# Performance work log

Measured on AMD Instinct MI355X. Metric: run time of the kernel, lower is better.

The kernel has to match this reference:

```python
import jax, jax.numpy as jnp
import numpy as np


def setup_inputs() -> dict:
    key = jax.random.key(0)
    ks = jax.random.split(key, 6)
    B, T, D, U = 128, 1024, 256, 256
    x = jax.random.normal(ks[0], (B, T, D), jnp.float32)
    s = lambda k, sh: jax.random.normal(k, sh, jnp.float32) * 0.05
    W_zr = s(ks[1], (D, 2 * U))
    U_zr = s(ks[2], (U, 2 * U))
    # bias_initializer: zeros for update gate, ones for reset gate
    b_zr = jnp.concatenate([jnp.zeros((U,), jnp.float32), jnp.ones((U,), jnp.float32)])
    W_h = s(ks[3], (D, U))
    U_h = s(ks[4], (U, U))
    b_h = jnp.zeros((U,), jnp.float32)
    return {"x": x, "W_zr": W_zr, "U_zr": U_zr, "b_zr": b_zr,
            "W_h": W_h, "U_h": U_h, "b_h": b_h}


def reference(x, W_zr, U_zr, b_zr, W_h, U_h, b_h):
    B, T, D = x.shape
    U = W_h.shape[1]
    # Precompute input-side projections for all timesteps (math-equivalent,
    # batches the per-step Dense(ip) matmuls into two big GEMMs).
    xz = jnp.einsum('btd,de->bte', x, W_zr)   # [B,T,2U]
    xh = jnp.einsum('btd,du->btu', x, W_h)    # [B,T,U]

    def step(h, inp):
        xz_t, xh_t = inp                       # [B,2U], [B,U]
        z = xz_t + h @ U_zr + b_zr
        Z = jax.nn.sigmoid(z[:, :U])           # update gate
        R = jax.nn.sigmoid(z[:, U:2 * U])      # reset gate
        S_ = jnp.tanh(xh_t + (R * h) @ U_h + b_h)
        h_new = (1.0 - Z) * h + Z * S_
        return h_new, None

    h0 = jnp.zeros((B, U), x.dtype)
    h_last, _ = jax.lax.scan(step, h0,
                             (jnp.swapaxes(xz, 0, 1), jnp.swapaxes(xh, 0, 1)))
    # return_sequence=False, return_states=False -> last hidden state [B,U]
    return h_last
```

## Files before the change

### kernel.cpp

```cpp
#include <hip/hip_runtime.h>
#include <hip/hip_bf16.h>
#include <cstdint>
#include <cstddef>

#define B_ 128
#define T_ 1024
#define D_ 256
#define U_ 256

typedef __bf16 bfrag __attribute__((ext_vector_type(8)));
typedef unsigned short us8 __attribute__((ext_vector_type(8)));
typedef unsigned short us4 __attribute__((ext_vector_type(4)));
typedef float f32x4 __attribute__((ext_vector_type(4)));

#define SC_ZR (-1.4426950408889634f)
#define SC_H  (2.8853900817779268f)

__device__ __forceinline__ unsigned short f2bf(float f) {
    unsigned int u = __builtin_bit_cast(unsigned int, f);
    unsigned int r = (u + 0x7fffu + ((u >> 16) & 1u)) >> 16;
    return (unsigned short)r;
}
__device__ __forceinline__ float bf2f(unsigned short h) {
    unsigned int u = ((unsigned int)h) << 16;
    return __builtin_bit_cast(float, u);
}
__device__ __forceinline__ unsigned int pk_bf16(float lo, float hi) {
    unsigned int d;
    asm("v_cvt_pk_bf16_f32 %0, %1, %2" : "=v"(d) : "v"(lo), "v"(hi));
    return d;
}
__device__ __forceinline__ unsigned int pk_hu(float lo, float hi) {
    unsigned int a = __builtin_bit_cast(unsigned int, lo) + 0x8000u;
    unsigned int b = __builtin_bit_cast(unsigned int, hi) + 0x8000u;
#if __has_builtin(__builtin_amdgcn_perm)
    return __builtin_amdgcn_perm(b, a, 0x07060302u);
#else
    return (b & 0xffff0000u) | (a >> 16);
#endif
}

#if __has_builtin(__builtin_amdgcn_exp2f)
__device__ __forceinline__ float fexp2(float x) { return __builtin_amdgcn_exp2f(x); }
#else
__device__ __forceinline__ float fexp2(float x) { return exp2f(x); }
#endif
#if __has_builtin(__builtin_amdgcn_rcpf)
__device__ __forceinline__ float frcp(float x) { return __builtin_amdgcn_rcpf(x); }
#else
__device__ __forceinline__ float frcp(float x) { return 1.0f / x; }
#endif

__device__ __forceinline__ float sigm_pre(float zp) {
    return frcp(1.0f + fexp2(zp));
}
__device__ __forceinline__ float tanh_pre(float sp) {
    return 1.0f - 2.0f * frcp(1.0f + fexp2(sp));
}

#define BARRIER_LGKM() asm volatile("s_waitcnt lgkmcnt(0)\n\ts_barrier" ::: "memory")

#define TSTR (32 * 768 * 4)
#define WTSZ (768 * 256)

__global__ __launch_bounds__(64) void wt_kernel(
    const float* __restrict__ Wzr, const float* __restrict__ Wh,
    unsigned short* __restrict__ Wt, int ncopies)
{
    const int c = blockIdx.x;
    const int lane = threadIdx.x;
    const float* Wp; int ldw, cc;
    if (c < 512) { Wp = Wzr; ldw = 512; cc = c; }
    else         { Wp = Wh;  ldw = 256; cc = c - 512; }
    const float sc = (c < 512) ? SC_ZR : SC_H;
    const int k0 = lane * 4;
    const float a = sc * Wp[(size_t)(k0 + 0) * ldw + cc];
    const float b = sc * Wp[(size_t)(k0 + 1) * ldw + cc];
    const float d = sc * Wp[(size_t)(k0 + 2) * ldw + cc];
    const float e = sc * Wp[(size_t)(k0 + 3) * ldw + cc];
    uint2 u; u.x = pk_bf16(a, b); u.y = pk_bf16(d, e);
    for (int r = 0; r < ncopies; ++r)
        *reinterpret_cast<uint2*>(&Wt[(size_t)r * WTSZ + (size_t)c * 256 + k0]) = u;
}

#define LPA 264

__global__ __launch_bounds__(256, 4) void proj_kernel(
    const float* __restrict__ x, const unsigned short* __restrict__ Wt,
    const float* __restrict__ bzr, const float* __restrict__ bh,
    unsigned short* __restrict__ xzh, size_t wtstride)
{
    const int tid  = threadIdx.x;
    const int lane = tid & 63;
    const int wv   = tid >> 6;
    const int q    = lane >> 4;
    const int c16  = lane & 15;
    const int bb = blockIdx.x >> 8;
    const int tb = blockIdx.x & 255;

    __shared__ __align__(16) unsigned short ldsA[64 * LPA];

    {
        const int r0 = wv * 16;
#pragma unroll
        for (int r = 0; r < 16; ++r) {
            const int row = r0 + r;
            const float* xr = x + (((size_t)(bb * 16 + (row & 15))) * T_
                                   + tb * 4 + (row >> 4)) * D_;
            f32x4 v = *reinterpret_cast<const f32x4*>(xr + lane * 4);
            uint2 u; u.x = pk_bf16(v[0], v[1]); u.y = pk_bf16(v[2], v[3]);
            *reinterpret_cast<uint2*>(&ldsA[row * LPA + lane * 4]) = u;
        }
    }
    __syncthreads();

    const int R0 = (wv >> 1) * 32;
    us8 af[2][8];
#pragma unroll
    for (int m2 = 0; m2 < 2; ++m2)
#pragma unroll
        for (int kk = 0; kk < 8; ++kk)
            af[m2][kk] = *reinterpret_cast<const us8*>(
                &ldsA[(R0 + m2 * 16 + c16) * LPA + kk * 32 + q * 8]);

    const int wn = wv & 1;
    const unsigned short* p0 = Wt + (size_t)bb * wtstride
                               + ((size_t)(wn * 32 + c16) * 256 + q * 8);
    const unsigned short* p1 = p0 + 16 * 256;

#pragma unroll 1
    for (int ch = 0; ch < 12; ++ch) {
        f32x4 acc[2][2] = {};
#pragma unroll
        for (int kk = 0; kk < 8; ++kk) {
            us8 w0 = *reinterpret_cast<const us8*>(p0 + kk * 32);
            us8 w1 = *reinterpret_cast<const us8*>(p1 + kk * 32);
#pragma unroll
            for (int m2 = 0; m2 < 2; ++m2) {
                acc[m2][0] = __builtin_amdgcn_mfma_f32_16x16x32_bf16(
                    __builtin_bit_cast(bfrag, af[m2][kk]), __builtin_bit_cast(bfrag, w0),
                    acc[m2][0], 0, 0, 0);
                acc[m2][1] = __builtin_amdgcn_mfma_f32_16x16x32_bf16(
                    __builtin_bit_cast(bfrag, af[m2][kk]), __builtin_bit_cast(bfrag, w1),
                    acc[m2][1], 0, 0, 0);
            }
        }
#pragma unroll
        for (int n2 = 0; n2 < 2; ++n2) {
            const int gcn = ch * 64 + wn * 32 + n2 * 16 + c16;
            const float bias = (gcn < 512) ? (SC_ZR * bzr[gcn])
                                           : (SC_H * bh[gcn - 512]);
#pragma unroll
            for (int m2 = 0; m2 < 2; ++m2) {
                const int t = tb * 4 + (wv >> 1) * 2 + m2;
                uint2 uu;
                uu.x = pk_bf16(acc[m2][n2][0] + bias, acc[m2][n2][1] + bias);
                uu.y = pk_bf16(acc[m2][n2][2] + bias, acc[m2][n2][3] + bias);
                *reinterpret_cast<uint2*>(
                    &xzh[(((size_t)t * 32 + bb * 4 + q) * 768 + gcn) * 4]) = uu;
            }
        }
        p0 += 64 * 256; p1 += 64 * 256;
    }
}

#define HBP 272

__global__ __launch_bounds__(512, 2) void gru_rec(
    const float* __restrict__ Uzr, const float* __restrict__ Uh,
    const unsigned short* __restrict__ xzh, float* __restrict__ out)
{
    const int tid  = threadIdx.x;
    const int lane = tid & 63;
    const int w    = tid >> 6;
    const int q    = lane >> 4;
    const int c16  = lane & 15;
    const int g    = blockIdx.x;

    __shared__ __align__(16) unsigned short hb[4 * HBP];
    __shared__ __align__(16) unsigned short rhb[4 * HBP];

    us8 wA[4][8];
#pragma unroll
    for (int nt = 0; nt < 4; ++nt) {
        const int col = (nt < 2) ? (w * 32 + nt * 16 + c16)
                                 : (256 + w * 32 + (nt - 2) * 16 + c16);
#pragma unroll
        for (int kk = 0; kk < 8; ++kk) {
            us8 v;
#pragma unroll
            for (int j = 0; j < 8; ++j) {
                const int kr = kk * 32 + q * 4 + (j >> 1) + 16 * (j & 1);
                v[j] = f2bf(SC_ZR * Uzr[(size_t)kr * 512 + col]);
            }
            wA[nt][kk] = v;
        }
    }
    us8 wB[2][8];
#pragma unroll
    for (int nt = 0; nt < 2; ++nt) {
        const int col = w * 32 + nt * 16 + c16;
#pragma unroll
        for (int kk = 0; kk < 8; ++kk) {
            us8 v;
#pragma unroll
            for (int j = 0; j < 8; ++j) {
                const int kr = kk * 32 + q * 4 + (j >> 1) + 16 * (j & 1);
                v[j] = f2bf(SC_H * Uh[(size_t)kr * 256 + col]);
            }
            wB[nt][kk] = v;
        }
    }

    for (int i = tid; i < 4 * HBP; i += 512) { hb[i] = 0; rhb[i] = 0; }
    __syncthreads();

    float h0 = 0.0f, h1 = 0.0f;

    size_t laneA[4], laneB[2];
#pragma unroll
    for (int nt = 0; nt < 4; ++nt) {
        const int col = (nt < 2) ? (w * 32 + nt * 16 + c16)
                                 : (256 + w * 32 + (nt - 2) * 16 + c16);
        laneA[nt] = ((size_t)g * 768 + col) * 4 + q;
    }
#pragma unroll
    for (int nt = 0; nt < 2; ++nt)
        laneB[nt] = ((size_t)g * 768 + 512 + w * 32 + nt * 16 + c16) * 4 + q;

    unsigned short ca[4], cxh[2];
#pragma unroll
    for (int nt = 0; nt < 4; ++nt) ca[nt] = xzh[laneA[nt]];
#pragma unroll
    for (int nt = 0; nt < 2; ++nt) cxh[nt] = xzh[laneB[nt]];

    size_t toff = TSTR;

    const int dwr = q * HBP + w * 32 + 2 * c16;
    const int ard = (c16 >> 2) * HBP + q * 8;

#pragma unroll 1
    for (int t = 0; t < T_; ++t) {
        unsigned short na[4], nxh[2];
#pragma unroll
        for (int nt = 0; nt < 4; ++nt) na[nt] = xzh[laneA[nt] + toff];
#pragma unroll
        for (int nt = 0; nt < 2; ++nt) nxh[nt] = xzh[laneB[nt] + toff];
        if (t < 1022) toff += TSTR;

        f32x4 acc[4];
#pragma unroll
        for (int nt = 0; nt < 4; ++nt) {
            const float v = bf2f(ca[nt]);
            acc[nt][0] = v; acc[nt][1] = v; acc[nt][2] = v; acc[nt][3] = v;
        }
#pragma unroll
        for (int kk = 0; kk < 8; ++kk) {
            bfrag af = __builtin_bit_cast(bfrag,
                *reinterpret_cast<const us8*>(&hb[ard + kk * 32]));
#pragma unroll
            for (int nt = 0; nt < 4; ++nt)
                acc[nt] = __builtin_amdgcn_mfma_f32_16x16x32_bf16(
                    af, __builtin_bit_cast(bfrag, wA[nt][kk]), acc[nt], 0, 0, 0);
        }
        {
            const float r0 = sigm_pre(acc[2][0]);
            const float r1 = sigm_pre(acc[3][0]);
            *reinterpret_cast<unsigned int*>(&rhb[dwr]) = pk_hu(r0 * h0, r1 * h1);
        }
        BARRIER_LGKM();

        f32x4 acc2[2];
#pragma unroll
        for (int nt = 0; nt < 2; ++nt) {
            const float v = bf2f(cxh[nt]);
            acc2[nt][0] = v; acc2[nt][1] = v; acc2[nt][2] = v; acc2[nt][3] = v;
        }
#pragma unroll
        for (int kk = 0; kk < 8; ++kk) {
            bfrag rf = __builtin_bit_cast(bfrag,
                *reinterpret_cast<const us8*>(&rhb[ard + kk * 32]));
#pragma unroll
            for (int nt = 0; nt < 2; ++nt)
                acc2[nt] = __builtin_amdgcn_mfma_f32_16x16x32_bf16(
                    rf, __builtin_bit_cast(bfrag, wB[nt][kk]), acc2[nt], 0, 0, 0);
        }
        {
            const float z0 = sigm_pre(acc[0][0]);
            const float z1 = sigm_pre(acc[1][0]);
            const float s0 = tanh_pre(acc2[0][0]);
            const float s1 = tanh_pre(acc2[1][0]);
            h0 = fmaf(z0, s0 - h0, h0);
            h1 = fmaf(z1, s1 - h1, h1);
            *reinterpret_cast<unsigned int*>(&hb[dwr]) = pk_hu(h0, h1);
        }
#pragma unroll
        for (int nt = 0; nt < 4; ++nt) ca[nt] = na[nt];
#pragma unroll
        for (int nt = 0; nt < 2; ++nt) cxh[nt] = nxh[nt];
        BARRIER_LGKM();
    }

    out[(size_t)(g * 4 + q) * 256 + w * 32 + c16] = h0;
    out[(size_t)(g * 4 + q) * 256 + w * 32 + 16 + c16] = h1;
}

extern "C" void kernel_launch(void* const* d_in, const int* in_sizes, int n_in,
                              void* d_out, int out_size, void* d_ws, size_t ws_size,
                              hipStream_t stream) {
    const float* x   = (const float*)d_in[0];
    const float* Wzr = (const float*)d_in[1];
    const float* Uzr = (const float*)d_in[2];
    const float* bzr = (const float*)d_in[3];
    const float* Wh  = (const float*)d_in[4];
    const float* Uh  = (const float*)d_in[5];
    const float* bh  = (const float*)d_in[6];
    float* out = (float*)d_out;

    const size_t xzhbytes = (size_t)T_ * TSTR * 2;
    const size_t wtbytes  = (size_t)WTSZ * 2;
    int ncopies = (ws_size >= xzhbytes + 8 * wtbytes) ? 8
                : (ws_size >= xzhbytes + wtbytes) ? 1 : 1;
    unsigned short* xzh = (unsigned short*)d_ws;
    unsigned short* Wt  = (unsigned short*)((char*)d_ws + xzhbytes);
    const size_t wtstride = (ncopies == 8) ? (size_t)WTSZ : 0;

    wt_kernel<<<dim3(768), dim3(64), 0, stream>>>(Wzr, Wh, Wt, ncopies);
    proj_kernel<<<dim3(2048), dim3(256), 0, stream>>>(x, Wt, bzr, bh, xzh, wtstride);
    gru_rec<<<dim3(32), dim3(512), 0, stream>>>(Uzr, Uh, xzh, out);
}
```

Baseline: 1.810 ms.

## Split MFMA accumulator chains, prefetch two steps ahead, and make xzh group-major

The recurrent loop is restructured into a two-step unrolled helper. Each matmul's K reduction is split across two independent accumulator sets to shorten the MFMA dependency chain. Projected inputs are now prefetched two timesteps ahead. The xzh buffer layout changes from time-major to batch-group-major so each workgroup reads its own contiguous region. The extra accumulators raise register pressure, and the proj kernel's writes now land at a strided layout.

```diff
diff --git a/kernel.cpp b/kernel.cpp
--- a/kernel.cpp
+++ b/kernel.cpp
@@ -60,8 +60,9 @@
 
 #define BARRIER_LGKM() asm volatile("s_waitcnt lgkmcnt(0)\n\ts_barrier" ::: "memory")
 
-#define TSTR (32 * 768 * 4)
-#define WTSZ (768 * 256)
+#define TSTR2 3072
+#define GSTR  ((size_t)T_ * TSTR2)
+#define WTSZ  (768 * 256)
 
 __global__ __launch_bounds__(64) void wt_kernel(
     const float* __restrict__ Wzr, const float* __restrict__ Wh,
@@ -157,7 +158,7 @@
                 uu.x = pk_bf16(acc[m2][n2][0] + bias, acc[m2][n2][1] + bias);
                 uu.y = pk_bf16(acc[m2][n2][2] + bias, acc[m2][n2][3] + bias);
                 *reinterpret_cast<uint2*>(
-                    &xzh[(((size_t)t * 32 + bb * 4 + q) * 768 + gcn) * 4]) = uu;
+                    &xzh[((((size_t)(bb * 4 + q)) * T_ + t) * 768 + gcn) * 4]) = uu;
             }
         }
         p0 += 64 * 256; p1 += 64 * 256;
@@ -165,6 +166,91 @@
 }
 
 #define HBP 272
+
+__device__ __forceinline__ void gru_step(
+    unsigned short (&ca)[4], unsigned short (&cxh)[2],
+    const us8 (&wA)[4][8], const us8 (&wB)[2][8],
+    const unsigned short* __restrict__ xzh,
+    const size_t (&laneA)[4], const size_t (&laneB)[2],
+    unsigned short* hb, unsigned short* rhb,
+    int ard, int dwr, float& h0, float& h1,
+    bool pf, size_t off)
+{
+    f32x4 accP[4], accQ[4];
+#pragma unroll
+    for (int nt = 0; nt < 4; ++nt) {
+        const float v = bf2f(ca[nt]);
+        accP[nt][0] = v; accP[nt][1] = v; accP[nt][2] = v; accP[nt][3] = v;
+        accQ[nt][0] = 0.f; accQ[nt][1] = 0.f; accQ[nt][2] = 0.f; accQ[nt][3] = 0.f;
+    }
+    f32x4 acc2P[2], acc2Q[2];
+#pragma unroll
+    for (int nt = 0; nt < 2; ++nt) {
+        const float v = bf2f(cxh[nt]);
+        acc2P[nt][0] = v; acc2P[nt][1] = v; acc2P[nt][2] = v; acc2P[nt][3] = v;
+        acc2Q[nt][0] = 0.f; acc2Q[nt][1] = 0.f; acc2Q[nt][2] = 0.f; acc2Q[nt][3] = 0.f;
+    }
+    if (pf) {
+#pragma unroll
+        for (int nt = 0; nt < 4; ++nt) ca[nt] = xzh[laneA[nt] + off];
+#pragma unroll
+        for (int nt = 0; nt < 2; ++nt) cxh[nt] = xzh[laneB[nt] + off];
+    }
+
+#pragma unroll
+    for (int kk = 0; kk < 4; ++kk) {
+        bfrag af = __builtin_bit_cast(bfrag,
+            *reinterpret_cast<const us8*>(&hb[ard + kk * 32]));
+#pragma unroll
+        for (int nt = 0; nt < 4; ++nt)
+            accP[nt] = __builtin_amdgcn_mfma_f32_16x16x32_bf16(
+                af, __builtin_bit_cast(bfrag, wA[nt][kk]), accP[nt], 0, 0, 0);
+    }
+#pragma unroll
+    for (int kk = 4; kk < 8; ++kk) {
+        bfrag af = __builtin_bit_cast(bfrag,
+            *reinterpret_cast<const us8*>(&hb[ard + kk * 32]));
+#pragma unroll
+        for (int nt = 0; nt < 4; ++nt)
+            accQ[nt] = __builtin_amdgcn_mfma_f32_16x16x32_bf16(
+                af, __builtin_bit_cast(bfrag, wA[nt][kk]), accQ[nt], 0, 0, 0);
+    }
+    {
+        const float r0 = sigm_pre(accP[2][0] + accQ[2][0]);
+        const float r1 = sigm_pre(accP[3][0] + accQ[3][0]);
+        *reinterpret_cast<unsigned int*>(&rhb[dwr]) = pk_hu(r0 * h0, r1 * h1);
+    }
+    BARRIER_LGKM();
+
+#pragma unroll
+    for (int kk = 0; kk < 4; ++kk) {
+        bfrag rf = __builtin_bit_cast(bfrag,
+            *reinterpret_cast<const us8*>(&rhb[ard + kk * 32]));
+#pragma unroll
+        for (int nt = 0; nt < 2; ++nt)
+            acc2P[nt] = __builtin_amdgcn_mfma_f32_16x16x32_bf16(
+                rf, __builtin_bit_cast(bfrag, wB[nt][kk]), acc2P[nt], 0, 0, 0);
+    }
+#pragma unroll
+    for (int kk = 4; kk < 8; ++kk) {
+        bfrag rf = __builtin_bit_cast(bfrag,
+            *reinterpret_cast<const us8*>(&rhb[ard + kk * 32]));
+#pragma unroll
+        for (int nt = 0; nt < 2; ++nt)
+            acc2Q[nt] = __builtin_amdgcn_mfma_f32_16x16x32_bf16(
+                rf, __builtin_bit_cast(bfrag, wB[nt][kk]), acc2Q[nt], 0, 0, 0);
+    }
+    {
+        const float z0 = sigm_pre(accP[0][0] + accQ[0][0]);
+        const float z1 = sigm_pre(accP[1][0] + accQ[1][0]);
+        const float s0 = tanh_pre(acc2P[0][0] + acc2Q[0][0]);
+        const float s1 = tanh_pre(acc2P[1][0] + acc2Q[1][0]);
+        h0 = fmaf(z0, s0 - h0, h0);
+        h1 = fmaf(z1, s1 - h1, h1);
+        *reinterpret_cast<unsigned int*>(&hb[dwr]) = pk_hu(h0, h1);
+    }
+    BARRIER_LGKM();
+}
 
 __global__ __launch_bounds__(512, 2) void gru_rec(
     const float* __restrict__ Uzr, const float* __restrict__ Uh,
@@ -222,83 +308,37 @@
     for (int nt = 0; nt < 4; ++nt) {
         const int col = (nt < 2) ? (w * 32 + nt * 16 + c16)
                                  : (256 + w * 32 + (nt - 2) * 16 + c16);
-        laneA[nt] = ((size_t)g * 768 + col) * 4 + q;
+        laneA[nt] = (size_t)g * GSTR + (size_t)col * 4 + q;
     }
 #pragma unroll
     for (int nt = 0; nt < 2; ++nt)
-        laneB[nt] = ((size_t)g * 768 + 512 + w * 32 + nt * 16 + c16) * 4 + q;
-
-    unsigned short ca[4], cxh[2];
-#pragma unroll
-    for (int nt = 0; nt < 4; ++nt) ca[nt] = xzh[laneA[nt]];
-#pragma unroll
-    for (int nt = 0; nt < 2; ++nt) cxh[nt] = xzh[laneB[nt]];
-
-    size_t toff = TSTR;
+        laneB[nt] = (size_t)g * GSTR
+                    + (size_t)(512 + w * 32 + nt * 16 + c16) * 4 + q;
+
+    unsigned short pa[4], ph[2], pb[4], qh[2];
+#pragma unroll
+    for (int nt = 0; nt < 4; ++nt) {
+        pa[nt] = xzh[laneA[nt]];
+        pb[nt] = xzh[laneA[nt] + TSTR2];
+    }
+#pragma unroll
+    for (int nt = 0; nt < 2; ++nt) {
+        ph[nt] = xzh[laneB[nt]];
+        qh[nt] = xzh[laneB[nt] + TSTR2];
+    }
 
     const int dwr = q * HBP + w * 32 + 2 * c16;
     const int ard = (c16 >> 2) * HBP + q * 8;
 
+    size_t off = 2 * (size_t)TSTR2;
 #pragma unroll 1
-    for (int t = 0; t < T_; ++t) {
-        unsigned short na[4], nxh[2];
-#pragma unroll
-        for (int nt = 0; nt < 4; ++nt) na[nt] = xzh[laneA[nt] + toff];
-#pragma unroll
-        for (int nt = 0; nt < 2; ++nt) nxh[nt] = xzh[laneB[nt] + toff];
-        if (t < 1022) toff += TSTR;
-
-        f32x4 acc[4];
-#pragma unroll
-        for (int nt = 0; nt < 4; ++nt) {
-            const float v = bf2f(ca[nt]);
-            acc[nt][0] = v; acc[nt][1] = v; acc[nt][2] = v; acc[nt][3] = v;
-        }
-#pragma unroll
-        for (int kk = 0; kk < 8; ++kk) {
-            bfrag af = __builtin_bit_cast(bfrag,
-                *reinterpret_cast<const us8*>(&hb[ard + kk * 32]));
-#pragma unroll
-            for (int nt = 0; nt < 4; ++nt)
-                acc[nt] = __builtin_amdgcn_mfma_f32_16x16x32_bf16(
-                    af, __builtin_bit_cast(bfrag, wA[nt][kk]), acc[nt], 0, 0, 0);
-        }
-        {
-            const float r0 = sigm_pre(acc[2][0]);
-            const float r1 = sigm_pre(acc[3][0]);
-            *reinterpret_cast<unsigned int*>(&rhb[dwr]) = pk_hu(r0 * h0, r1 * h1);
-        }
-        BARRIER_LGKM();
-
-        f32x4 acc2[2];
-#pragma unroll
-        for (int nt = 0; nt < 2; ++nt) {
-            const float v = bf2f(cxh[nt]);
-            acc2[nt][0] = v; acc2[nt][1] = v; acc2[nt][2] = v; acc2[nt][3] = v;
-        }
-#pragma unroll
-        for (int kk = 0; kk < 8; ++kk) {
-            bfrag rf = __builtin_bit_cast(bfrag,
-                *reinterpret_cast<const us8*>(&rhb[ard + kk * 32]));
-#pragma unroll
-            for (int nt = 0; nt < 2; ++nt)
-                acc2[nt] = __builtin_amdgcn_mfma_f32_16x16x32_bf16(
-                    rf, __builtin_bit_cast(bfrag, wB[nt][kk]), acc2[nt], 0, 0, 0);
-        }
-        {
-            const float z0 = sigm_pre(acc[0][0]);
-            const float z1 = sigm_pre(acc[1][0]);
-            const float s0 = tanh_pre(acc2[0][0]);
-            const float s1 = tanh_pre(acc2[1][0]);
-            h0 = fmaf(z0, s0 - h0, h0);
-            h1 = fmaf(z1, s1 - h1, h1);
-            *reinterpret_cast<unsigned int*>(&hb[dwr]) = pk_hu(h0, h1);
-        }
-#pragma unroll
-        for (int nt = 0; nt < 4; ++nt) ca[nt] = na[nt];
-#pragma unroll
-        for (int nt = 0; nt < 2; ++nt) cxh[nt] = nxh[nt];
-        BARRIER_LGKM();
+    for (int t = 0; t < T_; t += 2) {
+        const bool pf = (t < T_ - 2);
+        gru_step(pa, ph, wA, wB, xzh, laneA, laneB, hb, rhb,
+                 ard, dwr, h0, h1, pf, off);
+        gru_step(pb, qh, wA, wB, xzh, laneA, laneB, hb, rhb,
+                 ard, dwr, h0, h1, pf, off + TSTR2);
+        off += 2 * (size_t)TSTR2;
     }
 
     out[(size_t)(g * 4 + q) * 256 + w * 32 + c16] = h0;
@@ -317,7 +357,7 @@
     const float* bh  = (const float*)d_in[6];
     float* out = (float*)d_out;
 
-    const size_t xzhbytes = (size_t)T_ * TSTR * 2;
+    const size_t xzhbytes = (size_t)32 * GSTR * 2;
     const size_t wtbytes  = (size_t)WTSZ * 2;
     int ncopies = (ws_size >= xzhbytes + 8 * wtbytes) ? 8
                 : (ws_size >= xzhbytes + wtbytes) ? 1 : 1;
```

Measured after the change: 2.994 ms. 65.4% more time.
